# Optimization experiments

Hardware: AMD Instinct MI355X
Metric: run time of the kernel (lower is better)

Reference implementation:

```python
import jax, jax.numpy as jnp
import numpy as np

MAX_DISTANCE = 9          # search radius (pixels, at half resolution)
PAD_VAL = 1e10            # padding value; sigmoid saturates to 1 exactly as with 1e20,
                          # but avoids inf in fp32 squared sums (same output, safe grads)


def _offsets(m):
    k = 2 * m + 1
    offs = np.stack(np.meshgrid(np.arange(k), np.arange(k), indexing='ij'), -1)
    return jnp.asarray(offs.reshape(-1, 2))  # [K,2], row-major (dy, dx) like torch unfold


def _interp_matrix(out_size, in_size):
    # 1-D bilinear interpolation matrix, align_corners=True (matches F.interpolate)
    scale = (in_size - 1) / (out_size - 1)
    pos = jnp.arange(out_size, dtype=jnp.float32) * scale
    lo = jnp.clip(jnp.floor(pos).astype(jnp.int32), 0, in_size - 2)
    frac = pos - lo.astype(jnp.float32)
    rows = jnp.arange(out_size)
    M = jnp.zeros((out_size, in_size), jnp.float32)
    return M.at[rows, lo].add(1.0 - frac).at[rows, lo + 1].add(frac)


def _local_distances(query, prev, m):
    # local_pairwise_distances2 with MODEL_LOCAL_DOWNSAMPLE=True
    H, W, C = query.shape
    x = query.reshape(H // 2, 2, W // 2, 2, C).mean(axis=(1, 3))  # avg_pool2d 2x2
    y = prev.reshape(H // 2, 2, W // 2, 2, C).mean(axis=(1, 3))
    h, w = H // 2, W // 2
    ypad = jnp.pad(y, ((m, m), (m, m), (0, 0)), constant_values=PAD_VAL)
    offs = _offsets(m)

    def one(off):
        sl = jax.lax.dynamic_slice(ypad, (off[0], off[1], 0), (h, w, C))
        return jnp.sum((x - sl) ** 2, axis=-1)  # [h,w]

    d = jax.vmap(one)(offs)                      # [K,h,w]
    d = (jax.nn.sigmoid(d) - 0.5) * 2.0
    d = jnp.transpose(d, (1, 2, 0))              # [h,w,K]
    Mh = _interp_matrix(H, h)
    Mw = _interp_matrix(W, w)
    return jnp.einsum('Hh,Ww,hwk->HWk', Mh, Mw, d)  # bilinear upsample


def setup_inputs() -> dict:
    key = jax.random.key(0)
    k1, k2, k3 = jax.random.split(key, 3)
    H, W, C, n_objs = 96, 160, 100, 3
    return {
        'prev_frame_embedding': jax.random.normal(k1, (H, W, C), jnp.float32),
        'query_embedding': jax.random.normal(k2, (H, W, C), jnp.float32),
        'prev_frame_labels': jax.random.randint(k3, (H, W, 1), 0, n_objs).astype(jnp.int32),
        'gt_ids': jnp.arange(n_objs, dtype=jnp.int32),
    }


def reference(prev_frame_embedding, query_embedding, prev_frame_labels, gt_ids):
    m = MAX_DISTANCE
    H, W, _ = prev_frame_embedding.shape
    n = gt_ids.shape[0]
    d = _local_distances(query_embedding, prev_frame_embedding, m)  # [H,W,K]

    masks = prev_frame_labels == gt_ids[None, None, :]  # [H,W,n] bool
    mpad = jnp.pad(masks, ((m, m), (m, m), (0, 0)))      # pad False
    offs = _offsets(m)

    def one(off):
        return jax.lax.dynamic_slice(mpad, (off[0], off[1], 0), (H, W, n))

    om = jnp.transpose(jax.vmap(one)(offs), (1, 2, 0, 3))  # [H,W,K,n]
    d_masked = jnp.where(om, d[..., None], 1.0)
    dists = jnp.min(d_masked, axis=2)                      # [H,W,n]
    return dists.reshape(1, H, W, n, 1)
```

## Files before the change

kernel.cpp:

```cpp
#include <hip/hip_runtime.h>
#include <hip/hip_bf16.h>
#include <math.h>

#define HF 96
#define WF 160
#define CH 100
#define HH 48
#define HW 80
#define NPIX 3840
#define MD 9
#define KD 19
#define K2 361
#define NMAX 8

#define OFF_XT 0
#define OFF_YT (CH*NPIX)
#define OFF_XS (2*CH*NPIX)
#define OFF_YS (2*CH*NPIX + NPIX)
#define OFF_DH (2*CH*NPIX + 2*NPIX)

__global__ __launch_bounds__(256) void pool_kernel(
    const float* __restrict__ q, const float* __restrict__ p,
    float* __restrict__ Xt, float* __restrict__ Yt,
    float* __restrict__ xs, float* __restrict__ ys) {
  int w = threadIdx.x >> 6, L = threadIdx.x & 63;
  int pix = blockIdx.x * 4 + w;
  int i = pix / HW, j = pix - i * HW;
  int base = (2 * i) * WF * CH + (2 * j) * CH;
  float nx = 0.f, ny = 0.f;
  for (int c = L; c < CH; c += 64) {
    int b = base + c;
    float xv = 0.25f * (q[b] + q[b + CH] + q[b + WF * CH] + q[b + WF * CH + CH]);
    float yv = 0.25f * (p[b] + p[b + CH] + p[b + WF * CH] + p[b + WF * CH + CH]);
    Xt[c * NPIX + pix] = xv;
    Yt[c * NPIX + pix] = yv;
    nx = fmaf(xv, xv, nx);
    ny = fmaf(yv, yv, ny);
  }
  for (int s = 32; s > 0; s >>= 1) {
    nx += __shfl_down(nx, s);
    ny += __shfl_down(ny, s);
  }
  if (L == 0) { xs[pix] = nx; ys[pix] = ny; }
}

__global__ __launch_bounds__(256) void dist_kernel(
    const float* __restrict__ Xt, const float* __restrict__ Yt,
    const float* __restrict__ xs, const float* __restrict__ ys,
    __hip_bfloat16* __restrict__ dh2) {
  int pix = blockIdx.x * 256 + threadIdx.x;
  int u = blockIdx.y;
  int dy = u >> 1, h = u & 1;
  int i = pix / HW, j = pix - i * HW;
  int row = i + dy - MD;
  bool rowOK = (row >= 0 && row < HH);
  int rcl = row < 0 ? 0 : (row > HH - 1 ? HH - 1 : row);
  int cbase = j - MD + 10 * h;

  float acc[10];
#pragma unroll
  for (int d = 0; d < 10; ++d) acc[d] = 0.f;

  const float* xp = Xt + pix;
  const float* yp = Yt + rcl * HW + cbase;
  for (int c = 0; c < CH; ++c) {
    float xv = *xp;
#pragma unroll
    for (int d = 0; d < 10; ++d)
      acc[d] = fmaf(xv, yp[d], acc[d]);
    xp += NPIX; yp += NPIX;
  }

  float xss = xs[pix];
  const float* ysr = ys + rcl * HW;
  int nd = h ? 9 : 10;
  int kbase = dy * KD + 10 * h;
#pragma unroll
  for (int d = 0; d < 10; ++d) {
    if (d >= nd) break;
    int jj = cbase + d;
    bool ok = rowOK && (jj >= 0) && (jj < HW);
    int jcl = jj < 0 ? 0 : (jj > HW - 1 ? HW - 1 : jj);
    float s = xss + ysr[jcl] - 2.f * acc[d];
    float e = __expf(-s);
    float r = ok ? (1.f - e) / (1.f + e) : 1.0f;
    dh2[(kbase + d) * NPIX + pix] = __float2bfloat16(r);
  }
}

template <int N>
__global__ __launch_bounds__(1024) void upmin_kernel(
    const __hip_bfloat16* __restrict__ dh2, const int* __restrict__ labels,
    const int* __restrict__ gt, float* __restrict__ out) {
  int w = threadIdx.x >> 6;
  int lane = threadIdx.x & 63;
  int pixel = blockIdx.x * 64 + lane;
  int I = pixel / WF, J = pixel - I * WF;

  const float sy = (float)((HH - 1.0) / (HF - 1.0));
  const float sx = (float)((HW - 1.0) / (WF - 1.0));
  float py = (float)I * sy;
  int y0 = (int)floorf(py); if (y0 > HH - 2) y0 = HH - 2; if (y0 < 0) y0 = 0;
  float fy = py - (float)y0;
  float px = (float)J * sx;
  int x0 = (int)floorf(px); if (x0 > HW - 2) x0 = HW - 2; if (x0 < 0) x0 = 0;
  float fx = px - (float)x0;
  float w00 = (1.f - fy) * (1.f - fx), w01 = (1.f - fy) * fx;
  float w10 = fy * (1.f - fx),         w11 = fy * fx;
  int np00 = y0 * HW + x0;

  int gtl[N];
  float mins[N];
#pragma unroll
  for (int o = 0; o < N; ++o) { gtl[o] = gt[o]; mins[o] = 1.0f; }

  for (int k = w; k < K2; k += 16) {
    int dy = k / KD, dx = k - dy * KD;
    int P = I + dy - MD, Q = J + dx - MD;
    const __hip_bfloat16* dk = dh2 + k * NPIX + np00;
    float v = w00 * __bfloat162float(dk[0]) + w01 * __bfloat162float(dk[1]) +
              w10 * __bfloat162float(dk[HW]) + w11 * __bfloat162float(dk[HW + 1]);
    if (P >= 0 && P < HF && Q >= 0 && Q < WF) {
      int lab = labels[P * WF + Q];
#pragma unroll
      for (int o = 0; o < N; ++o)
        if (lab == gtl[o]) mins[o] = fminf(mins[o], v);
    }
  }

  __shared__ float mm[16][64][N];
#pragma unroll
  for (int o = 0; o < N; ++o) mm[w][lane][o] = mins[o];
  __syncthreads();
  if (w < 8) {
#pragma unroll
    for (int o = 0; o < N; ++o)
      mm[w][lane][o] = fminf(mm[w][lane][o], mm[w + 8][lane][o]);
  }
  __syncthreads();
  if (w < 4) {
#pragma unroll
    for (int o = 0; o < N; ++o)
      mm[w][lane][o] = fminf(mm[w][lane][o], mm[w + 4][lane][o]);
  }
  __syncthreads();
  if (w == 0) {
#pragma unroll
    for (int o = 0; o < N; ++o) {
      float m = fminf(fminf(mm[0][lane][o], mm[1][lane][o]),
                      fminf(mm[2][lane][o], mm[3][lane][o]));
      out[pixel * N + o] = m;
    }
  }
}

extern "C" void kernel_launch(void* const* d_in, const int* in_sizes, int n_in,
                              void* d_out, int out_size, void* d_ws, size_t ws_size,
                              hipStream_t stream) {
  const float* prev  = (const float*)d_in[0];
  const float* query = (const float*)d_in[1];
  const int* labels  = (const int*)d_in[2];
  const int* gt      = (const int*)d_in[3];
  int n = in_sizes[3];
  if (n > NMAX) n = NMAX;
  float* ws = (float*)d_ws;
  float* Xt = ws + OFF_XT;
  float* Yt = ws + OFF_YT;
  float* xs = ws + OFF_XS;
  float* ys = ws + OFF_YS;
  __hip_bfloat16* dh2 = (__hip_bfloat16*)(ws + OFF_DH);
  float* out = (float*)d_out;

  hipLaunchKernelGGL(pool_kernel, dim3(NPIX / 4), dim3(256), 0, stream,
                     query, prev, Xt, Yt, xs, ys);
  hipLaunchKernelGGL(dist_kernel, dim3(15, 38), dim3(256), 0, stream,
                     Xt, Yt, xs, ys, dh2);
  dim3 ug(HF * WF / 64), ub(1024);
  switch (n) {
    case 1: hipLaunchKernelGGL(upmin_kernel<1>, ug, ub, 0, stream, dh2, labels, gt, out); break;
    case 2: hipLaunchKernelGGL(upmin_kernel<2>, ug, ub, 0, stream, dh2, labels, gt, out); break;
    case 3: hipLaunchKernelGGL(upmin_kernel<3>, ug, ub, 0, stream, dh2, labels, gt, out); break;
    case 4: hipLaunchKernelGGL(upmin_kernel<4>, ug, ub, 0, stream, dh2, labels, gt, out); break;
    case 5: hipLaunchKernelGGL(upmin_kernel<5>, ug, ub, 0, stream, dh2, labels, gt, out); break;
    case 6: hipLaunchKernelGGL(upmin_kernel<6>, ug, ub, 0, stream, dh2, labels, gt, out); break;
    case 7: hipLaunchKernelGGL(upmin_kernel<7>, ug, ub, 0, stream, dh2, labels, gt, out); break;
    default: hipLaunchKernelGGL(upmin_kernel<8>, ug, ub, 0, stream, dh2, labels, gt, out); break;
  }
}
```

Measured before the change: 119.4 us.

## Share prev-row loads across two query rows and skip out-of-range rows in dist_kernel

Each thread of the distance kernel now computes two query pixels in vertically adjacent half-res rows. Both use the same prev-embedding row, so each loaded Y value feeds two FMAs and Y traffic per output is halved. Threads whose prev row falls outside the image write 1.0 directly and skip the channel loop. In exchange, register pressure doubles per thread and the grid is reshaped to 15x40 blocks of 128 threads.

```diff
diff --git a/kernel.cpp b/kernel.cpp
--- a/kernel.cpp
+++ b/kernel.cpp
@@ -44,47 +44,78 @@
   if (L == 0) { xs[pix] = nx; ys[pix] = ny; }
 }
 
-__global__ __launch_bounds__(256) void dist_kernel(
+__global__ __launch_bounds__(128) void dist_kernel(
     const float* __restrict__ Xt, const float* __restrict__ Yt,
     const float* __restrict__ xs, const float* __restrict__ ys,
     __hip_bfloat16* __restrict__ dh2) {
-  int pix = blockIdx.x * 256 + threadIdx.x;
+  int t = blockIdx.x * 128 + threadIdx.x;
   int u = blockIdx.y;
-  int dy = u >> 1, h = u & 1;
-  int i = pix / HW, j = pix - i * HW;
-  int row = i + dy - MD;
-  bool rowOK = (row >= 0 && row < HH);
-  int rcl = row < 0 ? 0 : (row > HH - 1 ? HH - 1 : row);
+  int dp = u >> 1, h = u & 1;
+  int ip = t / HW, j = t - ip * HW;
+  int iA = 2 * ip;
+  int pixA = iA * HW + j, pixB = pixA + HW;
+
+  bool doA = (dp < KD);
+  bool doB = (dp >= 1);
+  int r = iA + dp - MD;
+  bool rowOK = (r >= 0 && r < HH);
   int cbase = j - MD + 10 * h;
-
-  float acc[10];
-#pragma unroll
-  for (int d = 0; d < 10; ++d) acc[d] = 0.f;
-
-  const float* xp = Xt + pix;
-  const float* yp = Yt + rcl * HW + cbase;
+  int nd = h ? 9 : 10;
+  int kbA = dp * KD + 10 * h;
+  int kbB = (dp - 1) * KD + 10 * h;
+
+  if (!rowOK) {
+    __hip_bfloat16 one = __float2bfloat16(1.0f);
+#pragma unroll
+    for (int d = 0; d < 10; ++d) {
+      if (d >= nd) break;
+      if (doA) dh2[(kbA + d) * NPIX + pixA] = one;
+      if (doB) dh2[(kbB + d) * NPIX + pixB] = one;
+    }
+    return;
+  }
+
+  float accA[10], accB[10];
+#pragma unroll
+  for (int d = 0; d < 10; ++d) { accA[d] = 0.f; accB[d] = 0.f; }
+
+  const float* xpA = Xt + pixA;
+  const float* xpB = Xt + pixB;
+  const float* yp  = Yt + r * HW + cbase;
+#pragma unroll 2
   for (int c = 0; c < CH; ++c) {
-    float xv = *xp;
-#pragma unroll
-    for (int d = 0; d < 10; ++d)
-      acc[d] = fmaf(xv, yp[d], acc[d]);
-    xp += NPIX; yp += NPIX;
-  }
-
-  float xss = xs[pix];
-  const float* ysr = ys + rcl * HW;
-  int nd = h ? 9 : 10;
-  int kbase = dy * KD + 10 * h;
+    float xa = *xpA, xb = *xpB;
+#pragma unroll
+    for (int d = 0; d < 10; ++d) {
+      float yv = yp[d];
+      accA[d] = fmaf(xa, yv, accA[d]);
+      accB[d] = fmaf(xb, yv, accB[d]);
+    }
+    xpA += NPIX; xpB += NPIX; yp += NPIX;
+  }
+
+  float xssA = xs[pixA];
+  float xssB = xs[pixB];
+  const float* ysr = ys + r * HW;
 #pragma unroll
   for (int d = 0; d < 10; ++d) {
     if (d >= nd) break;
     int jj = cbase + d;
-    bool ok = rowOK && (jj >= 0) && (jj < HW);
+    bool okc = (jj >= 0) && (jj < HW);
     int jcl = jj < 0 ? 0 : (jj > HW - 1 ? HW - 1 : jj);
-    float s = xss + ysr[jcl] - 2.f * acc[d];
-    float e = __expf(-s);
-    float r = ok ? (1.f - e) / (1.f + e) : 1.0f;
-    dh2[(kbase + d) * NPIX + pix] = __float2bfloat16(r);
+    float yss = ysr[jcl];
+    if (doA) {
+      float s = xssA + yss - 2.f * accA[d];
+      float e = __expf(-s);
+      float rv = okc ? (1.f - e) / (1.f + e) : 1.0f;
+      dh2[(kbA + d) * NPIX + pixA] = __float2bfloat16(rv);
+    }
+    if (doB) {
+      float s = xssB + yss - 2.f * accB[d];
+      float e = __expf(-s);
+      float rv = okc ? (1.f - e) / (1.f + e) : 1.0f;
+      dh2[(kbB + d) * NPIX + pixB] = __float2bfloat16(rv);
+    }
   }
 }
 
@@ -173,7 +204,7 @@
 
   hipLaunchKernelGGL(pool_kernel, dim3(NPIX / 4), dim3(256), 0, stream,
                      query, prev, Xt, Yt, xs, ys);
-  hipLaunchKernelGGL(dist_kernel, dim3(15, 38), dim3(256), 0, stream,
+  hipLaunchKernelGGL(dist_kernel, dim3(1920 / 128, 40), dim3(128), 0, stream,
                      Xt, Yt, xs, ys, dh2);
   dim3 ug(HF * WF / 64), ub(1024);
   switch (n) {
```

Result: faster. 115.2 us (-3.5%).

## Restructure distance kernel to share Y rows across four query rows with split-channel reduction

Applied to the files above, without the earlier changes.

The distance kernel now has each thread compute four query rows that share the same padded Y row (r = 4*ipq + dp - MD), so each loaded Y value feeds four outputs instead of one. Packed f32x2 FMAs are used, and the channel dimension is split across four waves whose partial sums are reduced through shared memory. Fully out-of-range rows skip the dot product and write 1 directly. This cuts redundant Y loads and improves parallelism, at the cost of more registers, a shared-memory reduction and a barrier.

```diff
diff --git a/kernel.cpp b/kernel.cpp
--- a/kernel.cpp
+++ b/kernel.cpp
@@ -18,6 +18,8 @@
 #define OFF_XS (2*CH*NPIX)
 #define OFF_YS (2*CH*NPIX + NPIX)
 #define OFF_DH (2*CH*NPIX + 2*NPIX)
+
+typedef float f32x2 __attribute__((ext_vector_type(2)));
 
 __global__ __launch_bounds__(256) void pool_kernel(
     const float* __restrict__ q, const float* __restrict__ p,
@@ -44,47 +46,112 @@
   if (L == 0) { xs[pix] = nx; ys[pix] = ny; }
 }
 
-__global__ __launch_bounds__(256) void dist_kernel(
+__global__ __launch_bounds__(256, 3) void dist_kernel(
     const float* __restrict__ Xt, const float* __restrict__ Yt,
     const float* __restrict__ xs, const float* __restrict__ ys,
     __hip_bfloat16* __restrict__ dh2) {
-  int pix = blockIdx.x * 256 + threadIdx.x;
-  int u = blockIdx.y;
-  int dy = u >> 1, h = u & 1;
-  int i = pix / HW, j = pix - i * HW;
-  int row = i + dy - MD;
-  bool rowOK = (row >= 0 && row < HH);
-  int rcl = row < 0 ? 0 : (row > HH - 1 ? HH - 1 : row);
+  __shared__ float ex[3][64][41];
+  int il = threadIdx.x & 63;
+  int qtr = threadIdx.x >> 6;
+  int item = blockIdx.x * 64 + il;
+  int t = item % 960, u = item / 960;
+  int dp = u >> 1, h = u & 1;
+  int ipq = t / HW, j = t - ipq * HW;
+  int pix0 = ipq * (4 * HW) + j;
+  int r = 4 * ipq + dp - MD;
+  bool rowOK = (r >= 0 && r < HH);
   int cbase = j - MD + 10 * h;
-
-  float acc[10];
-#pragma unroll
-  for (int d = 0; d < 10; ++d) acc[d] = 0.f;
-
-  const float* xp = Xt + pix;
-  const float* yp = Yt + rcl * HW + cbase;
-  for (int c = 0; c < CH; ++c) {
-    float xv = *xp;
-#pragma unroll
-    for (int d = 0; d < 10; ++d)
-      acc[d] = fmaf(xv, yp[d], acc[d]);
-    xp += NPIX; yp += NPIX;
-  }
-
-  float xss = xs[pix];
-  const float* ysr = ys + rcl * HW;
   int nd = h ? 9 : 10;
-  int kbase = dy * KD + 10 * h;
+
+  f32x2 accA[10], accB[10];
+#pragma unroll
+  for (int d = 0; d < 10; ++d) { accA[d] = (f32x2){0.f, 0.f}; accB[d] = (f32x2){0.f, 0.f}; }
+
+  if (rowOK) {
+    const float* xp = Xt + (qtr * 25) * NPIX + pix0;
+    const float* yp = Yt + (qtr * 25) * NPIX + r * HW + cbase;
+#pragma unroll 5
+    for (int c = 0; c < 25; ++c) {
+      float x0 = xp[0], x1 = xp[HW], x2 = xp[2 * HW], x3 = xp[3 * HW];
+      f32x2 xA = {x0, x1}, xB = {x2, x3};
+#pragma unroll
+      for (int d = 0; d < 10; ++d) {
+        float yv = yp[d];
+        f32x2 yy = {yv, yv};
+        accA[d] = __builtin_elementwise_fma(xA, yy, accA[d]);
+        accB[d] = __builtin_elementwise_fma(xB, yy, accB[d]);
+      }
+      xp += NPIX; yp += NPIX;
+    }
+  }
+
+  if (qtr > 0 && rowOK) {
+#pragma unroll
+    for (int d = 0; d < 10; ++d) {
+      ex[qtr - 1][il][4 * d + 0] = accA[d].x;
+      ex[qtr - 1][il][4 * d + 1] = accA[d].y;
+      ex[qtr - 1][il][4 * d + 2] = accB[d].x;
+      ex[qtr - 1][il][4 * d + 3] = accB[d].y;
+    }
+  }
+  __syncthreads();
+  if (qtr != 0) return;
+
+  if (!rowOK) {
+    __hip_bfloat16 one = __float2bfloat16(1.0f);
+#pragma unroll
+    for (int rr = 0; rr < 4; ++rr) {
+      int dy = dp - rr;
+      if (dy < 0 || dy >= KD) continue;
+      int kb = dy * KD + 10 * h;
+      int pix = pix0 + rr * HW;
+#pragma unroll
+      for (int d = 0; d < 10; ++d) {
+        if (d >= nd) break;
+        dh2[(kb + d) * NPIX + pix] = one;
+      }
+    }
+    return;
+  }
+
+#pragma unroll
+  for (int q = 0; q < 3; ++q)
+#pragma unroll
+    for (int d = 0; d < 10; ++d) {
+      accA[d].x += ex[q][il][4 * d + 0];
+      accA[d].y += ex[q][il][4 * d + 1];
+      accB[d].x += ex[q][il][4 * d + 2];
+      accB[d].y += ex[q][il][4 * d + 3];
+    }
+
+  const float* ysr = ys + r * HW;
+  float yss[10];
+  bool okc[10];
 #pragma unroll
   for (int d = 0; d < 10; ++d) {
-    if (d >= nd) break;
     int jj = cbase + d;
-    bool ok = rowOK && (jj >= 0) && (jj < HW);
+    okc[d] = (jj >= 0) && (jj < HW);
     int jcl = jj < 0 ? 0 : (jj > HW - 1 ? HW - 1 : jj);
-    float s = xss + ysr[jcl] - 2.f * acc[d];
-    float e = __expf(-s);
-    float r = ok ? (1.f - e) / (1.f + e) : 1.0f;
-    dh2[(kbase + d) * NPIX + pix] = __float2bfloat16(r);
+    yss[d] = ysr[jcl];
+  }
+
+#pragma unroll
+  for (int rr = 0; rr < 4; ++rr) {
+    int dy = dp - rr;
+    if (dy < 0 || dy >= KD) continue;
+    int kb = dy * KD + 10 * h;
+    int pix = pix0 + rr * HW;
+    float xss = xs[pix];
+#pragma unroll
+    for (int d = 0; d < 10; ++d) {
+      if (d >= nd) break;
+      float a = (rr == 0) ? accA[d].x : (rr == 1) ? accA[d].y
+              : (rr == 2) ? accB[d].x : accB[d].y;
+      float s = xss + yss[d] - 2.f * a;
+      float e = __expf(-s);
+      float rv = okc[d] ? (1.f - e) / (1.f + e) : 1.0f;
+      dh2[(kb + d) * NPIX + pix] = __float2bfloat16(rv);
+    }
   }
 }
 
@@ -173,7 +240,7 @@
 
   hipLaunchKernelGGL(pool_kernel, dim3(NPIX / 4), dim3(256), 0, stream,
                      query, prev, Xt, Yt, xs, ys);
-  hipLaunchKernelGGL(dist_kernel, dim3(15, 38), dim3(256), 0, stream,
+  hipLaunchKernelGGL(dist_kernel, dim3(660), dim3(256), 0, stream,
                      Xt, Yt, xs, ys, dh2);
   dim3 ug(HF * WF / 64), ub(1024);
   switch (n) {
```

After: 104.7 us. 12.3% less time.
